# Kernel tuning notes

Measured on AMD Instinct MI355X. Metric: run time of the kernel, lower is better.

The kernel has to match this reference:

```python
import jax, jax.numpy as jnp
import numpy as np

N_NODES = 50000
N_EDGES = 800000
D_IN = 128
HID = [128, 64, 64]
N_CLASSES = 2
N_PROTO = 8
K = N_CLASSES * N_PROTO  # 16 = mlp_input_dim


def setup_inputs() -> dict:
    key = jax.random.key(0)
    ks = jax.random.split(key, 16)
    def lin(k, fi, fo):
        kw, kb = jax.random.split(k)
        s = 1.0 / np.sqrt(fi)
        return (jax.random.uniform(kw, (fi, fo), jnp.float32, -s, s),
                jax.random.uniform(kb, (fo,), jnp.float32, -s, s))
    W1, b1 = lin(ks[0], D_IN, HID[0])
    W2, b2 = lin(ks[1], HID[0], HID[1])
    W3, b3 = lin(ks[2], HID[1], HID[2])
    Wf0, bf0 = lin(ks[3], K, K // 2)
    Wf1, bf1 = lin(ks[4], K // 2, 1)
    return {
        'x': jax.random.normal(ks[5], (N_NODES, D_IN), jnp.float32),
        'edge_index': jax.random.randint(ks[6], (2, N_EDGES), 0, N_NODES, jnp.int64),
        'y': jax.random.randint(ks[7], (N_NODES,), 0, 2, jnp.int64),
        'W1': W1, 'b1': b1, 'W2': W2, 'b2': b2, 'W3': W3, 'b3': b3,
        'prototypes': jax.random.normal(ks[8], (N_CLASSES, N_PROTO, HID[2]), jnp.float32),
        'Wf0': Wf0, 'bf0': bf0, 'Wf1': Wf1, 'bf1': bf1,
    }


def reference(x, edge_index, y, W1, b1, W2, b2, W3, b3, prototypes, Wf0, bf0, Wf1, bf1):
    n = x.shape[0]
    loop = jnp.arange(n, dtype=edge_index.dtype)
    src = jnp.concatenate([edge_index[0], loop])  # A + I self loops (GCNConv default)
    dst = jnp.concatenate([edge_index[1], loop])
    deg = jax.ops.segment_sum(jnp.ones(src.shape[0], x.dtype), dst, num_segments=n)
    dinv = jax.lax.rsqrt(deg)  # deg >= 1 thanks to self loops
    enorm = dinv[src] * dinv[dst]  # sym-normalized edge weights

    def gcn(h, W, b):
        msg = (h @ W)[src] * enorm[:, None]  # gather + transform
        return jax.ops.segment_sum(msg, dst, num_segments=n) + b  # scatter-add

    h = jax.nn.relu(gcn(x, W1, b1))
    h = jax.nn.relu(gcn(h, W2, b2))
    h = jax.nn.relu(gcn(h, W3, b3))  # [n, 64]

    prot = prototypes.reshape(-1, prototypes.shape[-1])  # [K, 64]
    d2 = jnp.maximum(jnp.sum(h * h, -1, keepdims=True)
                     + jnp.sum(prot * prot, -1)[None, :]
                     - 2.0 * (h @ prot.T), 0.0)  # squared Euclidean [n, K]
    sim = jnp.log((d2 + 1.0) / (d2 + 1e-4))

    # MLPReadout, eval mode (dropout inactive), exact GELU like torch nn.GELU
    z = jax.nn.gelu(sim @ Wf0 + bf0, approximate=False)
    out = jax.nn.sigmoid(z @ Wf1 + bf1)
    return (out.squeeze(), y.astype(jnp.float32))
```

## Files before the change

### kernel.cpp

```cpp
#include <hip/hip_runtime.h>
#include <hip/hip_bf16.h>
#include <math.h>


typedef __attribute__((ext_vector_type(8))) short short8;
typedef __attribute__((ext_vector_type(4))) float f32x4;

#define BKT_SHIFT 5
#define BKT_NODES 32
#define EPB 2048
#define LCAP 1024
#define PREPN 28672
#define PREPB 112

__device__ __forceinline__ short f2bs(float x) {
    __hip_bfloat16 b = __float2bfloat16(x);
    return *reinterpret_cast<short*>(&b);
}
__device__ __forceinline__ float2 bpair(unsigned u) {
    float lo = __uint_as_float(u << 16);
    float hi = __uint_as_float(u & 0xffff0000u);
    return make_float2(lo, hi);
}
__device__ __forceinline__ unsigned packbf(float a, float b) {
    unsigned la = (unsigned)(unsigned short)f2bs(a);
    unsigned hb = (unsigned)(unsigned short)f2bs(b);
    return la | (hb << 16);
}

__device__ __forceinline__ void block_excl_scan(int* __restrict__ arr, int n, int t) {
    __shared__ int wsums[4];
    int lane = t & 63, wv = t >> 6;
    int carry = 0;
    for (int c0 = 0; c0 < n; c0 += 256) {
        int i = c0 + t;
        int v = (i < n) ? arr[i] : 0;
        int orig = v;
#pragma unroll
        for (int off = 1; off < 64; off <<= 1) {
            int u = __shfl_up(v, off, 64);
            if (lane >= off) v += u;
        }
        if (lane == 63) wsums[wv] = v;
        __syncthreads();
        int w0 = wsums[0], w1 = wsums[1], w2 = wsums[2], w3 = wsums[3];
        int woff = (wv > 0 ? w0 : 0) + (wv > 1 ? w1 : 0) + (wv > 2 ? w2 : 0);
        int tot = w0 + w1 + w2 + w3;
        __syncthreads();
        if (i < n) arr[i] = carry + woff + (v - orig);
        carry += tot;
    }
}


__global__ __launch_bounds__(256) void sort_local_kernel(const int* __restrict__ ei, int E,
                                                         int NB, int B,
                                                         int* __restrict__ glens,
                                                         int* __restrict__ gstart,
                                                         int* __restrict__ edge_sorted,
                                                         const float* __restrict__ W1,
                                                         const float* __restrict__ W2,
                                                         const float* __restrict__ W3,
                                                         __hip_bfloat16* __restrict__ Wp1,
                                                         __hip_bfloat16* __restrict__ Wp2,
                                                         __hip_bfloat16* __restrict__ Wp3) {
    int t = threadIdx.x;
    if ((int)blockIdx.x >= B) {
        int i = ((int)blockIdx.x - B) * 256 + t;
        if (i < 16384) {
            int k = i >> 7, n = i & 127;
            Wp1[(((k >> 3) * 128) + n) * 8 + (k & 7)] = __float2bfloat16(W1[i]);
        } else if (i < 24576) {
            int j = i - 16384;
            int k = j >> 6, n = j & 63;
            Wp2[(((k >> 3) * 64) + n) * 8 + (k & 7)] = __float2bfloat16(W2[j]);
        } else if (i < PREPN) {
            int j = i - 24576;
            int k = j >> 6, n = j & 63;
            Wp3[(((k >> 3) * 64) + n) * 8 + (k & 7)] = __float2bfloat16(W3[j]);
        }
        return;
    }
    extern __shared__ int lds[];
    int* hist  = lds;
    int* lbase = lds + NB;
    int* sortd = lds + 2 * NB;
    int blk = blockIdx.x;
    int e0 = blk * EPB;
    int cnt = E - e0;
    if (cnt > EPB) cnt = EPB;

    for (int i = t; i < NB; i += 256) hist[i] = 0;
    __syncthreads();
    for (int i = t; i < cnt; i += 256) {
        int dst = ei[E + e0 + i];
        atomicAdd(&hist[dst >> BKT_SHIFT], 1);
    }
    __syncthreads();
    for (int i = t; i < NB; i += 256) lbase[i] = hist[i];
    __syncthreads();
    block_excl_scan(lbase, NB, t);
    __syncthreads();
    for (int i = t; i < NB; i += 256) {
        glens[(size_t)blk * NB + i] = hist[i];
        gstart[(size_t)blk * NB + i] = lbase[i];
    }
    __syncthreads();
    for (int i = t; i < cnt; i += 256) {
        int src = ei[e0 + i];
        int dst = ei[E + e0 + i];
        int pos = atomicAdd(&lbase[dst >> BKT_SHIFT], 1);
        sortd[pos] = (src << BKT_SHIFT) | (dst & (BKT_NODES - 1));
    }
    __syncthreads();
    for (int i = t; i < cnt; i += 256) edge_sorted[e0 + i] = sortd[i];
}

__global__ __launch_bounds__(256) void csr_build_kernel(const int* __restrict__ edge_sorted,
                                                        const int* __restrict__ glens,
                                                        const int* __restrict__ gstart,
                                                        int NB, int B, int N,
                                                        int* __restrict__ row_beg,
                                                        int* __restrict__ row_end,
                                                        float* __restrict__ dinv,
                                                        int* __restrict__ csr) {
    __shared__ int lruns[512];
    __shared__ int loffs[512];
    __shared__ int sdeg[BKT_NODES];
    __shared__ int scur[BKT_NODES];
    __shared__ int raw[LCAP];
    __shared__ int srt[LCAP];
    int b = blockIdx.x;
    int t = threadIdx.x;

    for (int i = t; i < 512; i += 256) {
        int v = (i < B) ? glens[(size_t)i * NB + b] : 0;
        lruns[i] = v;
        loffs[i] = v;
    }
    if (t < BKT_NODES) sdeg[t] = 0;
    __syncthreads();
    block_excl_scan(loffs, B, t);
    __syncthreads();
    int cnt = loffs[B - 1] + lruns[B - 1];
    if (cnt > LCAP) cnt = LCAP;

    for (int r = t; r < B; r += 256) {
        int len = lruns[r];
        if (len) {
            int off = loffs[r];
            int st = r * EPB + gstart[(size_t)r * NB + b];
            for (int k = 0; k < len; ++k) {
                int p = off + k;
                if (p < LCAP) raw[p] = edge_sorted[st + k];
            }
        }
    }
    __syncthreads();

    for (int i = t; i < cnt; i += 256) atomicAdd(&sdeg[raw[i] & (BKT_NODES - 1)], 1);
    __syncthreads();
    int base = b * LCAP;
    if (t < BKT_NODES) {
        int ssum = 0;
        for (int i = 0; i < t; ++i) ssum += sdeg[i];
        scur[t] = ssum;
        int node = b * BKT_NODES + t;
        if (node < N) {
            row_beg[node] = base + ssum;
            row_end[node] = base + ssum + sdeg[t];
            dinv[node] = rsqrtf((float)(sdeg[t] + 1));
        }
    }
    __syncthreads();
    for (int i = t; i < cnt; i += 256) {
        int p = raw[i];
        int pos = atomicAdd(&scur[p & (BKT_NODES - 1)], 1);
        srt[pos] = p >> BKT_SHIFT;
    }
    __syncthreads();
    for (int i = t; i < cnt; i += 256) csr[base + i] = srt[i];
}


template <int DI, int DO, bool AF32>
__global__ __launch_bounds__(256) void mfma_gemm_kernel(const void* __restrict__ Av,
                                                        const __hip_bfloat16* __restrict__ Wp,
                                                        const float* __restrict__ dinv,
                                                        __hip_bfloat16* __restrict__ C, int N) {
    constexpr int NT = DO / 16;
    int t = threadIdx.x;
    int wave = t >> 6, lane = t & 63;
    int q = lane >> 4, l16 = lane & 15;
    int rbase = blockIdx.x * 64 + wave * 16;
    int row = rbase + l16;
    int rowc = row < N ? row : N - 1;

    f32x4 acc[NT];
#pragma unroll
    for (int i = 0; i < NT; ++i) acc[i] = (f32x4){0.f, 0.f, 0.f, 0.f};

#pragma unroll
    for (int kt = 0; kt < DI / 32; ++kt) {
        int k0 = kt * 32 + q * 8;
        short8 afrag;
        if (AF32) {
            const float* A = (const float*)Av;
            const float* ap = A + (size_t)rowc * DI + k0;
            float4 lo = *(const float4*)ap;
            float4 hi = *(const float4*)(ap + 4);
            afrag[0] = f2bs(lo.x); afrag[1] = f2bs(lo.y);
            afrag[2] = f2bs(lo.z); afrag[3] = f2bs(lo.w);
            afrag[4] = f2bs(hi.x); afrag[5] = f2bs(hi.y);
            afrag[6] = f2bs(hi.z); afrag[7] = f2bs(hi.w);
        } else {
            const __hip_bfloat16* A = (const __hip_bfloat16*)Av;
            afrag = *(const short8*)(A + (size_t)rowc * DI + k0);
        }
        const short8* wrow = (const short8*)(Wp + (size_t)(kt * 4 + q) * DO * 8);
#pragma unroll
        for (int tt = 0; tt < NT; ++tt) {
            short8 bfrag = wrow[tt * 16 + l16];
            acc[tt] = __builtin_amdgcn_mfma_f32_16x16x32_bf16(afrag, bfrag, acc[tt], 0, 0, 0);
        }
    }
#pragma unroll
    for (int r = 0; r < 4; ++r) {
        int gr = rbase + q * 4 + r;
        if (gr < N) {
            float dv = dinv[gr];
#pragma unroll
            for (int tt = 0; tt < NT; ++tt)
                C[(size_t)gr * DO + tt * 16 + l16] = __float2bfloat16(acc[tt][r] * dv);
        }
    }
}


__global__ __launch_bounds__(256) void agg128_kernel(const uint4* __restrict__ tmp,
                                                     const float* __restrict__ bias,
                                                     const float* __restrict__ dinv,
                                                     const int* __restrict__ row_beg,
                                                     const int* __restrict__ row_end,
                                                     const int* __restrict__ csr_src,
                                                     uint4* __restrict__ outp, int N) {
    int lane = threadIdx.x & 63;
    int q = lane >> 4, sub = lane & 15;
    int node = blockIdx.x * 4 + (threadIdx.x >> 6);
    if (node >= N) return;
    float dvi = dinv[node];
    float a0 = 0, a1 = 0, a2 = 0, a3 = 0, a4 = 0, a5 = 0, a6 = 0, a7 = 0;
    if (q == 0) {
        uint4 sv = tmp[(size_t)node * 16 + sub];
        float2 p0 = bpair(sv.x), p1 = bpair(sv.y), p2 = bpair(sv.z), p3 = bpair(sv.w);
        a0 = p0.x; a1 = p0.y; a2 = p1.x; a3 = p1.y;
        a4 = p2.x; a5 = p2.y; a6 = p3.x; a7 = p3.y;
    }
    int beg = row_beg[node], end = row_end[node];
    for (int j = beg; j < end; j += 64) {
        int m = end - j;
        if (m > 64) m = 64;
        int s = (lane < m) ? csr_src[j + lane] : 0;
        int iters = (m + 3) >> 2;
        for (int k = 0; k < iters; ++k) {
            int e = 4 * k + q;
            int ec = (e < m) ? e : 0;
            int sk = __shfl(s, ec, 64);
            uint4 v = tmp[(size_t)sk * 16 + sub];
            if (e < m) {
                float2 p0 = bpair(v.x), p1 = bpair(v.y), p2 = bpair(v.z), p3 = bpair(v.w);
                a0 += p0.x; a1 += p0.y; a2 += p1.x; a3 += p1.y;
                a4 += p2.x; a5 += p2.y; a6 += p3.x; a7 += p3.y;
            }
        }
    }
    a0 += __shfl_xor(a0, 16, 64); a1 += __shfl_xor(a1, 16, 64);
    a2 += __shfl_xor(a2, 16, 64); a3 += __shfl_xor(a3, 16, 64);
    a4 += __shfl_xor(a4, 16, 64); a5 += __shfl_xor(a5, 16, 64);
    a6 += __shfl_xor(a6, 16, 64); a7 += __shfl_xor(a7, 16, 64);
    a0 += __shfl_xor(a0, 32, 64); a1 += __shfl_xor(a1, 32, 64);
    a2 += __shfl_xor(a2, 32, 64); a3 += __shfl_xor(a3, 32, 64);
    a4 += __shfl_xor(a4, 32, 64); a5 += __shfl_xor(a5, 32, 64);
    a6 += __shfl_xor(a6, 32, 64); a7 += __shfl_xor(a7, 32, 64);
    if (q == 0) {
        float4 b0 = *(const float4*)&bias[sub * 8];
        float4 b1 = *(const float4*)&bias[sub * 8 + 4];
        uint4 o;
        o.x = packbf(fmaxf(dvi * a0 + b0.x, 0.f), fmaxf(dvi * a1 + b0.y, 0.f));
        o.y = packbf(fmaxf(dvi * a2 + b0.z, 0.f), fmaxf(dvi * a3 + b0.w, 0.f));
        o.z = packbf(fmaxf(dvi * a4 + b1.x, 0.f), fmaxf(dvi * a5 + b1.y, 0.f));
        o.w = packbf(fmaxf(dvi * a6 + b1.z, 0.f), fmaxf(dvi * a7 + b1.w, 0.f));
        outp[(size_t)node * 16 + sub] = o;
    }
}

__global__ __launch_bounds__(256) void agg64_kernel(const uint4* __restrict__ tmp,
                                                    const float* __restrict__ bias,
                                                    const float* __restrict__ dinv,
                                                    const int* __restrict__ row_beg,
                                                    const int* __restrict__ row_end,
                                                    const int* __restrict__ csr_src,
                                                    uint4* __restrict__ outp, int N) {
    int lane = threadIdx.x & 63;
    int o8 = lane >> 3, sub = lane & 7;
    int node = blockIdx.x * 4 + (threadIdx.x >> 6);
    if (node >= N) return;
    float dvi = dinv[node];
    float a0 = 0, a1 = 0, a2 = 0, a3 = 0, a4 = 0, a5 = 0, a6 = 0, a7 = 0;
    if (o8 == 0) {
        uint4 sv = tmp[(size_t)node * 8 + sub];
        float2 p0 = bpair(sv.x), p1 = bpair(sv.y), p2 = bpair(sv.z), p3 = bpair(sv.w);
        a0 = p0.x; a1 = p0.y; a2 = p1.x; a3 = p1.y;
        a4 = p2.x; a5 = p2.y; a6 = p3.x; a7 = p3.y;
    }
    int beg = row_beg[node], end = row_end[node];
    for (int j = beg; j < end; j += 64) {
        int m = end - j;
        if (m > 64) m = 64;
        int s = (lane < m) ? csr_src[j + lane] : 0;
        int iters = (m + 7) >> 3;
        for (int k = 0; k < iters; ++k) {
            int e = 8 * k + o8;
            int ec = (e < m) ? e : 0;
            int sk = __shfl(s, ec, 64);
            uint4 v = tmp[(size_t)sk * 8 + sub];
            if (e < m) {
                float2 p0 = bpair(v.x), p1 = bpair(v.y), p2 = bpair(v.z), p3 = bpair(v.w);
                a0 += p0.x; a1 += p0.y; a2 += p1.x; a3 += p1.y;
                a4 += p2.x; a5 += p2.y; a6 += p3.x; a7 += p3.y;
            }
        }
    }
    a0 += __shfl_xor(a0, 8, 64); a1 += __shfl_xor(a1, 8, 64);
    a2 += __shfl_xor(a2, 8, 64); a3 += __shfl_xor(a3, 8, 64);
    a4 += __shfl_xor(a4, 8, 64); a5 += __shfl_xor(a5, 8, 64);
    a6 += __shfl_xor(a6, 8, 64); a7 += __shfl_xor(a7, 8, 64);
    a0 += __shfl_xor(a0, 16, 64); a1 += __shfl_xor(a1, 16, 64);
    a2 += __shfl_xor(a2, 16, 64); a3 += __shfl_xor(a3, 16, 64);
    a4 += __shfl_xor(a4, 16, 64); a5 += __shfl_xor(a5, 16, 64);
    a6 += __shfl_xor(a6, 16, 64); a7 += __shfl_xor(a7, 16, 64);
    a0 += __shfl_xor(a0, 32, 64); a1 += __shfl_xor(a1, 32, 64);
    a2 += __shfl_xor(a2, 32, 64); a3 += __shfl_xor(a3, 32, 64);
    a4 += __shfl_xor(a4, 32, 64); a5 += __shfl_xor(a5, 32, 64);
    a6 += __shfl_xor(a6, 32, 64); a7 += __shfl_xor(a7, 32, 64);
    if (o8 == 0) {
        float4 b0 = *(const float4*)&bias[sub * 8];
        float4 b1 = *(const float4*)&bias[sub * 8 + 4];
        uint4 o;
        o.x = packbf(fmaxf(dvi * a0 + b0.x, 0.f), fmaxf(dvi * a1 + b0.y, 0.f));
        o.y = packbf(fmaxf(dvi * a2 + b0.z, 0.f), fmaxf(dvi * a3 + b0.w, 0.f));
        o.z = packbf(fmaxf(dvi * a4 + b1.x, 0.f), fmaxf(dvi * a5 + b1.y, 0.f));
        o.w = packbf(fmaxf(dvi * a6 + b1.z, 0.f), fmaxf(dvi * a7 + b1.w, 0.f));
        outp[(size_t)node * 8 + sub] = o;
    }
}


__global__ __launch_bounds__(256) void head_kernel(const unsigned* __restrict__ h,
                                                   const float* __restrict__ protos,
                                                   const float* __restrict__ Wf0,
                                                   const float* __restrict__ bf0,
                                                   const float* __restrict__ Wf1,
                                                   const float* __restrict__ bf1,
                                                   const int* __restrict__ y,
                                                   float* __restrict__ out, int N) {
    __shared__ float Hl[64 * 65];
    __shared__ float Pl[16 * 65];
    __shared__ float hh[64];
    __shared__ float pp[16];
    __shared__ float sim[64 * 17];
    __shared__ float Wf0l[128];
    __shared__ float bf0l[8];
    __shared__ float Wf1l[8];
    __shared__ float bf1l;
    int t = threadIdx.x;
    int n0 = blockIdx.x * 64;

    for (int idx = t; idx < 64 * 32; idx += 256) {
        int r = idx >> 5, c = idx & 31;
        int g = n0 + r;
        unsigned u = (g < N) ? h[(size_t)g * 32 + c] : 0u;
        float2 v = bpair(u);
        Hl[r * 65 + 2 * c] = v.x;
        Hl[r * 65 + 2 * c + 1] = v.y;
    }
    for (int idx = t; idx < 16 * 64; idx += 256) {
        int r = idx >> 6, c = idx & 63;
        Pl[r * 65 + c] = protos[idx];
    }
    if (t < 128) Wf0l[t] = Wf0[t];
    if (t < 8) { bf0l[t] = bf0[t]; Wf1l[t] = Wf1[t]; }
    if (t == 0) bf1l = bf1[0];
    __syncthreads();

    if (t < 64) {
        float s = 0.0f;
        for (int k = 0; k < 64; ++k) { float v = Hl[t * 65 + k]; s += v * v; }
        hh[t] = s;
    } else if (t < 80) {
        int p = t - 64;
        float s = 0.0f;
        for (int k = 0; k < 64; ++k) { float v = Pl[p * 65 + k]; s += v * v; }
        pp[p] = s;
    }
    __syncthreads();

    {
        int node = t & 63;
        int p4 = (t >> 6) * 4;
        float d0 = 0, d1 = 0, d2 = 0, d3 = 0;
        for (int k = 0; k < 64; ++k) {
            float hv = Hl[node * 65 + k];
            d0 += hv * Pl[(p4 + 0) * 65 + k];
            d1 += hv * Pl[(p4 + 1) * 65 + k];
            d2 += hv * Pl[(p4 + 2) * 65 + k];
            d3 += hv * Pl[(p4 + 3) * 65 + k];
        }
        float hhv = hh[node];
        float dd[4] = {d0, d1, d2, d3};
#pragma unroll
        for (int j = 0; j < 4; ++j) {
            float q = hhv + pp[p4 + j] - 2.0f * dd[j];
            q = q > 0.0f ? q : 0.0f;
            sim[node * 17 + p4 + j] = logf((q + 1.0f) / (q + 1e-4f));
        }
    }
    __syncthreads();

    if (t < 64) {
        int g = n0 + t;
        if (g < N) {
            float zacc = bf1l;
#pragma unroll
            for (int o = 0; o < 8; ++o) {
                float s = bf0l[o];
#pragma unroll
                for (int i2 = 0; i2 < 16; ++i2) s += sim[t * 17 + i2] * Wf0l[i2 * 8 + o];
                float gz = 0.5f * s * (1.0f + erff(s * 0.70710678118654752f));
                zacc += gz * Wf1l[o];
            }
            out[g] = 1.0f / (1.0f + expf(-zacc));
        }
    } else if (t < 128) {
        int g = n0 + (t - 64);
        if (g < N) out[N + g] = (float)y[g];
    }
}


extern "C" void kernel_launch(void* const* d_in, const int* in_sizes, int n_in,
                              void* d_out, int out_size, void* d_ws, size_t ws_size,
                              hipStream_t stream) {
    const float* x   = (const float*)d_in[0];
    const int*   ei  = (const int*)d_in[1];
    const int*   y   = (const int*)d_in[2];
    const float* W1  = (const float*)d_in[3];
    const float* b1  = (const float*)d_in[4];
    const float* W2  = (const float*)d_in[5];
    const float* b2  = (const float*)d_in[6];
    const float* W3  = (const float*)d_in[7];
    const float* b3  = (const float*)d_in[8];
    const float* pr  = (const float*)d_in[9];
    const float* Wf0 = (const float*)d_in[10];
    const float* bf0 = (const float*)d_in[11];
    const float* Wf1 = (const float*)d_in[12];
    const float* bf1 = (const float*)d_in[13];
    float* outp = (float*)d_out;

    const int N = in_sizes[2];
    const int E = in_sizes[1] / 2;
    const int NB = (N + BKT_NODES - 1) / BKT_NODES;
    const int B = (E + EPB - 1) / EPB;

    char* w = (char*)d_ws;
    auto carve = [&](size_t bytes) {
        char* p = w;
        w += (bytes + 511) & ~(size_t)511;
        return p;
    };
    int*   glens   = (int*)carve((size_t)B * NB * 4);
    int*   gstart  = (int*)carve((size_t)B * NB * 4);
    int*   esort   = (int*)carve((size_t)B * EPB * 4);
    int*   row_beg = (int*)carve((size_t)N * 4);
    int*   row_end = (int*)carve((size_t)N * 4);
    float* dinv    = (float*)carve((size_t)N * 4);
    int*   csr     = (int*)carve((size_t)NB * LCAP * 4);
    __hip_bfloat16* Wp1 = (__hip_bfloat16*)carve(16384 * 2);
    __hip_bfloat16* Wp2 = (__hip_bfloat16*)carve(8192 * 2);
    __hip_bfloat16* Wp3 = (__hip_bfloat16*)carve(4096 * 2);
    __hip_bfloat16* bufT = (__hip_bfloat16*)carve((size_t)N * 128 * 2);
    __hip_bfloat16* bufH = (__hip_bfloat16*)carve((size_t)N * 128 * 2);

    size_t sort_lds = (size_t)(2 * NB + EPB) * 4;

    sort_local_kernel<<<B + PREPB, 256, sort_lds, stream>>>(ei, E, NB, B, glens, gstart, esort,
                                                            W1, W2, W3, Wp1, Wp2, Wp3);
    csr_build_kernel<<<NB, 256, 0, stream>>>(esort, glens, gstart, NB, B, N,
                                             row_beg, row_end, dinv, csr);

    mfma_gemm_kernel<128, 128, true><<<(N + 63) / 64, 256, 0, stream>>>(x, Wp1, dinv, bufT, N);
    agg128_kernel<<<(N + 3) / 4, 256, 0, stream>>>((const uint4*)bufT, b1, dinv, row_beg, row_end,
                                                   csr, (uint4*)bufH, N);
    mfma_gemm_kernel<128, 64, false><<<(N + 63) / 64, 256, 0, stream>>>(bufH, Wp2, dinv, bufT, N);
    agg64_kernel<<<(N + 3) / 4, 256, 0, stream>>>((const uint4*)bufT, b2, dinv, row_beg, row_end,
                                                  csr, (uint4*)bufH, N);
    mfma_gemm_kernel<64, 64, false><<<(N + 63) / 64, 256, 0, stream>>>(bufH, Wp3, dinv, bufT, N);
    agg64_kernel<<<(N + 3) / 4, 256, 0, stream>>>((const uint4*)bufT, b3, dinv, row_beg, row_end,
                                                  csr, (uint4*)bufH, N);
    head_kernel<<<(N + 63) / 64, 256, 0, stream>>>((const unsigned*)bufH, pr, Wf0, bf0, Wf1, bf1,
                                                   y, outp, N);
}
```

Measured before the change: 246.1 us.

## Fuse GEMMs into aggregation kernels and overlap layer-1 GEMM with CSR build

The layer-1 GEMM now runs in the same launch as the CSR build, which lets it proceed without dinv; the source-side normalization moves into the first aggregation. The layer-2 and layer-3 transforms are fused into the preceding aggregation kernels as fp32 LDS matvecs, and the head is fused into the final aggregation. This drops kernel launches and the intermediate activation round trips through memory. The cost is that the small GEMMs move from MFMA to scalar FMA, with W2 and W3 read from global memory by every block, and the head now runs only 4 nodes per block with little parallelism.

Measured after the change: 317.4 us. 29.0% more time.

```diff
diff --git a/kernel.cpp b/kernel.cpp
--- a/kernel.cpp
+++ b/kernel.cpp
@@ -10,8 +10,6 @@
 #define BKT_NODES 32
 #define EPB 2048
 #define LCAP 1024
-#define PREPN 28672
-#define PREPB 112
 
 __device__ __forceinline__ short f2bs(float x) {
     __hip_bfloat16 b = __float2bfloat16(x);
@@ -21,11 +19,6 @@
     float lo = __uint_as_float(u << 16);
     float hi = __uint_as_float(u & 0xffff0000u);
     return make_float2(lo, hi);
-}
-__device__ __forceinline__ unsigned packbf(float a, float b) {
-    unsigned la = (unsigned)(unsigned short)f2bs(a);
-    unsigned hb = (unsigned)(unsigned short)f2bs(b);
-    return la | (hb << 16);
 }
 
 __device__ __forceinline__ void block_excl_scan(int* __restrict__ arr, int n, int t) {
@@ -53,31 +46,19 @@
 }
 
 
-__global__ __launch_bounds__(256) void sort_local_kernel(const int* __restrict__ ei, int E,
-                                                         int NB, int B,
-                                                         int* __restrict__ glens,
-                                                         int* __restrict__ gstart,
-                                                         int* __restrict__ edge_sorted,
-                                                         const float* __restrict__ W1,
-                                                         const float* __restrict__ W2,
-                                                         const float* __restrict__ W3,
-                                                         __hip_bfloat16* __restrict__ Wp1,
-                                                         __hip_bfloat16* __restrict__ Wp2,
-                                                         __hip_bfloat16* __restrict__ Wp3) {
+__global__ __launch_bounds__(256) void sort_w1_kernel(const int* __restrict__ ei, int E,
+                                                      int NB, int B,
+                                                      int* __restrict__ glens,
+                                                      int* __restrict__ gstart,
+                                                      int* __restrict__ edge_sorted,
+                                                      const float* __restrict__ W1,
+                                                      __hip_bfloat16* __restrict__ Wp1) {
     int t = threadIdx.x;
     if ((int)blockIdx.x >= B) {
         int i = ((int)blockIdx.x - B) * 256 + t;
         if (i < 16384) {
             int k = i >> 7, n = i & 127;
             Wp1[(((k >> 3) * 128) + n) * 8 + (k & 7)] = __float2bfloat16(W1[i]);
-        } else if (i < 24576) {
-            int j = i - 16384;
-            int k = j >> 6, n = j & 63;
-            Wp2[(((k >> 3) * 64) + n) * 8 + (k & 7)] = __float2bfloat16(W2[j]);
-        } else if (i < PREPN) {
-            int j = i - 24576;
-            int k = j >> 6, n = j & 63;
-            Wp3[(((k >> 3) * 64) + n) * 8 + (k & 7)] = __float2bfloat16(W3[j]);
         }
         return;
     }
@@ -116,14 +97,58 @@
     for (int i = t; i < cnt; i += 256) edge_sorted[e0 + i] = sortd[i];
 }
 
-__global__ __launch_bounds__(256) void csr_build_kernel(const int* __restrict__ edge_sorted,
+
+__global__ __launch_bounds__(256) void csr_gemm1_kernel(const int* __restrict__ edge_sorted,
                                                         const int* __restrict__ glens,
                                                         const int* __restrict__ gstart,
                                                         int NB, int B, int N,
                                                         int* __restrict__ row_beg,
                                                         int* __restrict__ row_end,
                                                         float* __restrict__ dinv,
-                                                        int* __restrict__ csr) {
+                                                        int* __restrict__ csr,
+                                                        const float* __restrict__ X,
+                                                        const __hip_bfloat16* __restrict__ Wp1,
+                                                        __hip_bfloat16* __restrict__ T1) {
+    int t = threadIdx.x;
+    if ((int)blockIdx.x >= NB) {
+        int bid = (int)blockIdx.x - NB;
+        int wave = t >> 6, lane = t & 63;
+        int q = lane >> 4, l16 = lane & 15;
+        int rbase = bid * 64 + wave * 16;
+        int row = rbase + l16;
+        int rowc = row < N ? row : N - 1;
+        f32x4 acc[8];
+#pragma unroll
+        for (int i = 0; i < 8; ++i) acc[i] = (f32x4){0.f, 0.f, 0.f, 0.f};
+#pragma unroll
+        for (int kt = 0; kt < 4; ++kt) {
+            int k0 = kt * 32 + q * 8;
+            const float* ap = X + (size_t)rowc * 128 + k0;
+            float4 lo = *(const float4*)ap;
+            float4 hi = *(const float4*)(ap + 4);
+            short8 afrag;
+            afrag[0] = f2bs(lo.x); afrag[1] = f2bs(lo.y);
+            afrag[2] = f2bs(lo.z); afrag[3] = f2bs(lo.w);
+            afrag[4] = f2bs(hi.x); afrag[5] = f2bs(hi.y);
+            afrag[6] = f2bs(hi.z); afrag[7] = f2bs(hi.w);
+            const short8* wrow = (const short8*)(Wp1 + (size_t)(kt * 4 + q) * 128 * 8);
+#pragma unroll
+            for (int tt = 0; tt < 8; ++tt) {
+                short8 bfrag = wrow[tt * 16 + l16];
+                acc[tt] = __builtin_amdgcn_mfma_f32_16x16x32_bf16(afrag, bfrag, acc[tt], 0, 0, 0);
+            }
+        }
+#pragma unroll
+        for (int r = 0; r < 4; ++r) {
+            int gr = rbase + q * 4 + r;
+            if (gr < N) {
+#pragma unroll
+                for (int tt = 0; tt < 8; ++tt)
+                    T1[(size_t)gr * 128 + tt * 16 + l16] = __float2bfloat16(acc[tt][r]);
+            }
+        }
+        return;
+    }
     __shared__ int lruns[512];
     __shared__ int loffs[512];
     __shared__ int sdeg[BKT_NODES];
@@ -131,7 +156,6 @@
     __shared__ int raw[LCAP];
     __shared__ int srt[LCAP];
     int b = blockIdx.x;
-    int t = threadIdx.x;
 
     for (int i = t; i < 512; i += 256) {
         int v = (i < B) ? glens[(size_t)i * NB + b] : 0;
@@ -157,7 +181,6 @@
         }
     }
     __syncthreads();
-
     for (int i = t; i < cnt; i += 256) atomicAdd(&sdeg[raw[i] & (BKT_NODES - 1)], 1);
     __syncthreads();
     int base = b * LCAP;
@@ -183,94 +206,46 @@
 }
 
 
-template <int DI, int DO, bool AF32>
-__global__ __launch_bounds__(256) void mfma_gemm_kernel(const void* __restrict__ Av,
-                                                        const __hip_bfloat16* __restrict__ Wp,
+__global__ __launch_bounds__(256) void agg128_g2_kernel(const uint4* __restrict__ T1,
+                                                        const float* __restrict__ b1,
                                                         const float* __restrict__ dinv,
-                                                        __hip_bfloat16* __restrict__ C, int N) {
-    constexpr int NT = DO / 16;
+                                                        const int* __restrict__ row_beg,
+                                                        const int* __restrict__ row_end,
+                                                        const int* __restrict__ csr,
+                                                        const float* __restrict__ W2,
+                                                        __hip_bfloat16* __restrict__ T2, int N) {
+    __shared__ float h1[4][128];
     int t = threadIdx.x;
-    int wave = t >> 6, lane = t & 63;
-    int q = lane >> 4, l16 = lane & 15;
-    int rbase = blockIdx.x * 64 + wave * 16;
-    int row = rbase + l16;
-    int rowc = row < N ? row : N - 1;
-
-    f32x4 acc[NT];
-#pragma unroll
-    for (int i = 0; i < NT; ++i) acc[i] = (f32x4){0.f, 0.f, 0.f, 0.f};
-
-#pragma unroll
-    for (int kt = 0; kt < DI / 32; ++kt) {
-        int k0 = kt * 32 + q * 8;
-        short8 afrag;
-        if (AF32) {
-            const float* A = (const float*)Av;
-            const float* ap = A + (size_t)rowc * DI + k0;
-            float4 lo = *(const float4*)ap;
-            float4 hi = *(const float4*)(ap + 4);
-            afrag[0] = f2bs(lo.x); afrag[1] = f2bs(lo.y);
-            afrag[2] = f2bs(lo.z); afrag[3] = f2bs(lo.w);
-            afrag[4] = f2bs(hi.x); afrag[5] = f2bs(hi.y);
-            afrag[6] = f2bs(hi.z); afrag[7] = f2bs(hi.w);
-        } else {
-            const __hip_bfloat16* A = (const __hip_bfloat16*)Av;
-            afrag = *(const short8*)(A + (size_t)rowc * DI + k0);
-        }
-        const short8* wrow = (const short8*)(Wp + (size_t)(kt * 4 + q) * DO * 8);
-#pragma unroll
-        for (int tt = 0; tt < NT; ++tt) {
-            short8 bfrag = wrow[tt * 16 + l16];
-            acc[tt] = __builtin_amdgcn_mfma_f32_16x16x32_bf16(afrag, bfrag, acc[tt], 0, 0, 0);
-        }
-    }
-#pragma unroll
-    for (int r = 0; r < 4; ++r) {
-        int gr = rbase + q * 4 + r;
-        if (gr < N) {
-            float dv = dinv[gr];
-#pragma unroll
-            for (int tt = 0; tt < NT; ++tt)
-                C[(size_t)gr * DO + tt * 16 + l16] = __float2bfloat16(acc[tt][r] * dv);
-        }
-    }
-}
-
-
-__global__ __launch_bounds__(256) void agg128_kernel(const uint4* __restrict__ tmp,
-                                                     const float* __restrict__ bias,
-                                                     const float* __restrict__ dinv,
-                                                     const int* __restrict__ row_beg,
-                                                     const int* __restrict__ row_end,
-                                                     const int* __restrict__ csr_src,
-                                                     uint4* __restrict__ outp, int N) {
-    int lane = threadIdx.x & 63;
+    int lane = t & 63, wv = t >> 6;
     int q = lane >> 4, sub = lane & 15;
-    int node = blockIdx.x * 4 + (threadIdx.x >> 6);
-    if (node >= N) return;
-    float dvi = dinv[node];
+    int node = blockIdx.x * 4 + wv;
+    int nd = node < N ? node : N - 1;
+    float dvi = dinv[nd];
     float a0 = 0, a1 = 0, a2 = 0, a3 = 0, a4 = 0, a5 = 0, a6 = 0, a7 = 0;
     if (q == 0) {
-        uint4 sv = tmp[(size_t)node * 16 + sub];
+        uint4 sv = T1[(size_t)nd * 16 + sub];
         float2 p0 = bpair(sv.x), p1 = bpair(sv.y), p2 = bpair(sv.z), p3 = bpair(sv.w);
-        a0 = p0.x; a1 = p0.y; a2 = p1.x; a3 = p1.y;
-        a4 = p2.x; a5 = p2.y; a6 = p3.x; a7 = p3.y;
-    }
-    int beg = row_beg[node], end = row_end[node];
+        a0 = dvi * p0.x; a1 = dvi * p0.y; a2 = dvi * p1.x; a3 = dvi * p1.y;
+        a4 = dvi * p2.x; a5 = dvi * p2.y; a6 = dvi * p3.x; a7 = dvi * p3.y;
+    }
+    int beg = row_beg[nd], end = row_end[nd];
     for (int j = beg; j < end; j += 64) {
         int m = end - j;
         if (m > 64) m = 64;
-        int s = (lane < m) ? csr_src[j + lane] : 0;
+        int s = 0;
+        float dv = 0.0f;
+        if (lane < m) { s = csr[j + lane]; dv = dinv[s]; }
         int iters = (m + 3) >> 2;
         for (int k = 0; k < iters; ++k) {
             int e = 4 * k + q;
             int ec = (e < m) ? e : 0;
             int sk = __shfl(s, ec, 64);
-            uint4 v = tmp[(size_t)sk * 16 + sub];
+            float dk = __shfl(dv, ec, 64);
+            uint4 v = T1[(size_t)sk * 16 + sub];
             if (e < m) {
                 float2 p0 = bpair(v.x), p1 = bpair(v.y), p2 = bpair(v.z), p3 = bpair(v.w);
-                a0 += p0.x; a1 += p0.y; a2 += p1.x; a3 += p1.y;
-                a4 += p2.x; a5 += p2.y; a6 += p3.x; a7 += p3.y;
+                a0 += dk * p0.x; a1 += dk * p0.y; a2 += dk * p1.x; a3 += dk * p1.y;
+                a4 += dk * p2.x; a5 += dk * p2.y; a6 += dk * p3.x; a7 += dk * p3.y;
             }
         }
     }
@@ -283,47 +258,60 @@
     a4 += __shfl_xor(a4, 32, 64); a5 += __shfl_xor(a5, 32, 64);
     a6 += __shfl_xor(a6, 32, 64); a7 += __shfl_xor(a7, 32, 64);
     if (q == 0) {
-        float4 b0 = *(const float4*)&bias[sub * 8];
-        float4 b1 = *(const float4*)&bias[sub * 8 + 4];
-        uint4 o;
-        o.x = packbf(fmaxf(dvi * a0 + b0.x, 0.f), fmaxf(dvi * a1 + b0.y, 0.f));
-        o.y = packbf(fmaxf(dvi * a2 + b0.z, 0.f), fmaxf(dvi * a3 + b0.w, 0.f));
-        o.z = packbf(fmaxf(dvi * a4 + b1.x, 0.f), fmaxf(dvi * a5 + b1.y, 0.f));
-        o.w = packbf(fmaxf(dvi * a6 + b1.z, 0.f), fmaxf(dvi * a7 + b1.w, 0.f));
-        outp[(size_t)node * 16 + sub] = o;
-    }
-}
-
-__global__ __launch_bounds__(256) void agg64_kernel(const uint4* __restrict__ tmp,
-                                                    const float* __restrict__ bias,
-                                                    const float* __restrict__ dinv,
-                                                    const int* __restrict__ row_beg,
-                                                    const int* __restrict__ row_end,
-                                                    const int* __restrict__ csr_src,
-                                                    uint4* __restrict__ outp, int N) {
-    int lane = threadIdx.x & 63;
+        float4 bb0 = *(const float4*)&b1[sub * 8];
+        float4 bb1 = *(const float4*)&b1[sub * 8 + 4];
+        h1[wv][sub * 8 + 0] = fmaxf(dvi * a0 + bb0.x, 0.f);
+        h1[wv][sub * 8 + 1] = fmaxf(dvi * a1 + bb0.y, 0.f);
+        h1[wv][sub * 8 + 2] = fmaxf(dvi * a2 + bb0.z, 0.f);
+        h1[wv][sub * 8 + 3] = fmaxf(dvi * a3 + bb0.w, 0.f);
+        h1[wv][sub * 8 + 4] = fmaxf(dvi * a4 + bb1.x, 0.f);
+        h1[wv][sub * 8 + 5] = fmaxf(dvi * a5 + bb1.y, 0.f);
+        h1[wv][sub * 8 + 6] = fmaxf(dvi * a6 + bb1.z, 0.f);
+        h1[wv][sub * 8 + 7] = fmaxf(dvi * a7 + bb1.w, 0.f);
+    }
+    __syncthreads();
+    int nd2 = t >> 6, c = t & 63;
+    float acc = 0.0f;
+#pragma unroll 4
+    for (int k = 0; k < 128; ++k) acc += h1[nd2][k] * W2[k * 64 + c];
+    int gn = blockIdx.x * 4 + nd2;
+    if (gn < N) T2[(size_t)gn * 64 + c] = __float2bfloat16(dinv[gn] * acc);
+}
+
+
+__global__ __launch_bounds__(256) void agg64_g3_kernel(const uint4* __restrict__ T2,
+                                                       const float* __restrict__ b2,
+                                                       const float* __restrict__ dinv,
+                                                       const int* __restrict__ row_beg,
+                                                       const int* __restrict__ row_end,
+                                                       const int* __restrict__ csr,
+                                                       const float* __restrict__ W3,
+                                                       __hip_bfloat16* __restrict__ T3, int N) {
+    __shared__ float h2[4][64];
+    int t = threadIdx.x;
+    int lane = t & 63, wv = t >> 6;
     int o8 = lane >> 3, sub = lane & 7;
-    int node = blockIdx.x * 4 + (threadIdx.x >> 6);
-    if (node >= N) return;
-    float dvi = dinv[node];
+    int node = blockIdx.x * 4 + wv;
+    int nd = node < N ? node : N - 1;
+    float dvi = dinv[nd];
     float a0 = 0, a1 = 0, a2 = 0, a3 = 0, a4 = 0, a5 = 0, a6 = 0, a7 = 0;
     if (o8 == 0) {
-        uint4 sv = tmp[(size_t)node * 8 + sub];
+        uint4 sv = T2[(size_t)nd * 8 + sub];
         float2 p0 = bpair(sv.x), p1 = bpair(sv.y), p2 = bpair(sv.z), p3 = bpair(sv.w);
         a0 = p0.x; a1 = p0.y; a2 = p1.x; a3 = p1.y;
         a4 = p2.x; a5 = p2.y; a6 = p3.x; a7 = p3.y;
     }
-    int beg = row_beg[node], end = row_end[node];
+    int beg = row_beg[nd], end = row_end[nd];
     for (int j = beg; j < end; j += 64) {
         int m = end - j;
         if (m > 64) m = 64;
-        int s = (lane < m) ? csr_src[j + lane] : 0;
+        int s = (lane < m) ? csr[j + lane] : 0;
         int iters = (m + 7) >> 3;
         for (int k = 0; k < iters; ++k) {
             int e = 8 * k + o8;
             int ec = (e < m) ? e : 0;
             int sk = __shfl(s, ec, 64);
-            uint4 v = tmp[(size_t)sk * 8 + sub];
+            uint4 v = T2[(size_t)sk * 8 + sub];
             if (e < m) {
                 float2 p0 = bpair(v.x), p1 = bpair(v.y), p2 = bpair(v.z), p3 = bpair(v.w);
                 a0 += p0.x; a1 += p0.y; a2 += p1.x; a3 += p1.y;
@@ -331,119 +319,142 @@
             }
         }
     }
-    a0 += __shfl_xor(a0, 8, 64); a1 += __shfl_xor(a1, 8, 64);
-    a2 += __shfl_xor(a2, 8, 64); a3 += __shfl_xor(a3, 8, 64);
-    a4 += __shfl_xor(a4, 8, 64); a5 += __shfl_xor(a5, 8, 64);
-    a6 += __shfl_xor(a6, 8, 64); a7 += __shfl_xor(a7, 8, 64);
-    a0 += __shfl_xor(a0, 16, 64); a1 += __shfl_xor(a1, 16, 64);
-    a2 += __shfl_xor(a2, 16, 64); a3 += __shfl_xor(a3, 16, 64);
-    a4 += __shfl_xor(a4, 16, 64); a5 += __shfl_xor(a5, 16, 64);
-    a6 += __shfl_xor(a6, 16, 64); a7 += __shfl_xor(a7, 16, 64);
-    a0 += __shfl_xor(a0, 32, 64); a1 += __shfl_xor(a1, 32, 64);
-    a2 += __shfl_xor(a2, 32, 64); a3 += __shfl_xor(a3, 32, 64);
-    a4 += __shfl_xor(a4, 32, 64); a5 += __shfl_xor(a5, 32, 64);
-    a6 += __shfl_xor(a6, 32, 64); a7 += __shfl_xor(a7, 32, 64);
+#pragma unroll
+    for (int off = 8; off <= 32; off <<= 1) {
+        a0 += __shfl_xor(a0, off, 64); a1 += __shfl_xor(a1, off, 64);
+        a2 += __shfl_xor(a2, off, 64); a3 += __shfl_xor(a3, off, 64);
+        a4 += __shfl_xor(a4, off, 64); a5 += __shfl_xor(a5, off, 64);
+        a6 += __shfl_xor(a6, off, 64); a7 += __shfl_xor(a7, off, 64);
+    }
     if (o8 == 0) {
-        float4 b0 = *(const float4*)&bias[sub * 8];
-        float4 b1 = *(const float4*)&bias[sub * 8 + 4];
-        uint4 o;
-        o.x = packbf(fmaxf(dvi * a0 + b0.x, 0.f), fmaxf(dvi * a1 + b0.y, 0.f));
-        o.y = packbf(fmaxf(dvi * a2 + b0.z, 0.f), fmaxf(dvi * a3 + b0.w, 0.f));
-        o.z = packbf(fmaxf(dvi * a4 + b1.x, 0.f), fmaxf(dvi * a5 + b1.y, 0.f));
-        o.w = packbf(fmaxf(dvi * a6 + b1.z, 0.f), fmaxf(dvi * a7 + b1.w, 0.f));
-        outp[(size_t)node * 8 + sub] = o;
-    }
-}
-
-
-__global__ __launch_bounds__(256) void head_kernel(const unsigned* __restrict__ h,
-                                                   const float* __restrict__ protos,
-                                                   const float* __restrict__ Wf0,
-                                                   const float* __restrict__ bf0,
-                                                   const float* __restrict__ Wf1,
-                                                   const float* __restrict__ bf1,
-                                                   const int* __restrict__ y,
-                                                   float* __restrict__ out, int N) {
-    __shared__ float Hl[64 * 65];
-    __shared__ float Pl[16 * 65];
-    __shared__ float hh[64];
+        float4 bb0 = *(const float4*)&b2[sub * 8];
+        float4 bb1 = *(const float4*)&b2[sub * 8 + 4];
+        h2[wv][sub * 8 + 0] = fmaxf(dvi * a0 + bb0.x, 0.f);
+        h2[wv][sub * 8 + 1] = fmaxf(dvi * a1 + bb0.y, 0.f);
+        h2[wv][sub * 8 + 2] = fmaxf(dvi * a2 + bb0.z, 0.f);
+        h2[wv][sub * 8 + 3] = fmaxf(dvi * a3 + bb0.w, 0.f);
+        h2[wv][sub * 8 + 4] = fmaxf(dvi * a4 + bb1.x, 0.f);
+        h2[wv][sub * 8 + 5] = fmaxf(dvi * a5 + bb1.y, 0.f);
+        h2[wv][sub * 8 + 6] = fmaxf(dvi * a6 + bb1.z, 0.f);
+        h2[wv][sub * 8 + 7] = fmaxf(dvi * a7 + bb1.w, 0.f);
+    }
+    __syncthreads();
+    int nd2 = t >> 6, c = t & 63;
+    float acc = 0.0f;
+#pragma unroll 4
+    for (int k = 0; k < 64; ++k) acc += h2[nd2][k] * W3[k * 64 + c];
+    int gn = blockIdx.x * 4 + nd2;
+    if (gn < N) T3[(size_t)gn * 64 + c] = __float2bfloat16(dinv[gn] * acc);
+}
+
+
+__global__ __launch_bounds__(256) void agg64_head_kernel(const uint4* __restrict__ T3,
+                                                         const float* __restrict__ b3,
+                                                         const float* __restrict__ dinv,
+                                                         const int* __restrict__ row_beg,
+                                                         const int* __restrict__ row_end,
+                                                         const int* __restrict__ csr,
+                                                         const float* __restrict__ protos,
+                                                         const float* __restrict__ Wf0,
+                                                         const float* __restrict__ bf0,
+                                                         const float* __restrict__ Wf1,
+                                                         const float* __restrict__ bf1,
+                                                         const int* __restrict__ y,
+                                                         float* __restrict__ out, int N) {
+    __shared__ float h3[4][65];
+    __shared__ float Pl[16][65];
+    __shared__ float hh[4];
     __shared__ float pp[16];
-    __shared__ float sim[64 * 17];
-    __shared__ float Wf0l[128];
-    __shared__ float bf0l[8];
-    __shared__ float Wf1l[8];
-    __shared__ float bf1l;
+    __shared__ float sim[4][16];
     int t = threadIdx.x;
-    int n0 = blockIdx.x * 64;
-
-    for (int idx = t; idx < 64 * 32; idx += 256) {
-        int r = idx >> 5, c = idx & 31;
-        int g = n0 + r;
-        unsigned u = (g < N) ? h[(size_t)g * 32 + c] : 0u;
-        float2 v = bpair(u);
-        Hl[r * 65 + 2 * c] = v.x;
-        Hl[r * 65 + 2 * c + 1] = v.y;
-    }
-    for (int idx = t; idx < 16 * 64; idx += 256) {
-        int r = idx >> 6, c = idx & 63;
-        Pl[r * 65 + c] = protos[idx];
-    }
-    if (t < 128) Wf0l[t] = Wf0[t];
-    if (t < 8) { bf0l[t] = bf0[t]; Wf1l[t] = Wf1[t]; }
-    if (t == 0) bf1l = bf1[0];
-    __syncthreads();
-
+    int lane = t & 63, wv = t >> 6;
+    int o8 = lane >> 3, sub = lane & 7;
+    int node = blockIdx.x * 4 + wv;
+    int nd = node < N ? node : N - 1;
+    float dvi = dinv[nd];
+
+    for (int idx = t; idx < 1024; idx += 256) Pl[idx >> 6][idx & 63] = protos[idx];
+
+    float a0 = 0, a1 = 0, a2 = 0, a3 = 0, a4 = 0, a5 = 0, a6 = 0, a7 = 0;
+    if (o8 == 0) {
+        uint4 sv = T3[(size_t)nd * 8 + sub];
+        float2 p0 = bpair(sv.x), p1 = bpair(sv.y), p2 = bpair(sv.z), p3 = bpair(sv.w);
+        a0 = p0.x; a1 = p0.y; a2 = p1.x; a3 = p1.y;
+        a4 = p2.x; a5 = p2.y; a6 = p3.x; a7 = p3.y;
+    }
+    int beg = row_beg[nd], end = row_end[nd];
+    for (int j = beg; j < end; j += 64) {
+        int m = end - j;
+        if (m > 64) m = 64;
+        int s = (lane < m) ? csr[j + lane] : 0;
+        int iters = (m + 7) >> 3;
+        for (int k = 0; k < iters; ++k) {
+            int e = 8 * k + o8;
+            int ec = (e < m) ? e : 0;
+            int sk = __shfl(s, ec, 64);
+            uint4 v = T3[(size_t)sk * 8 + sub];
+            if (e < m) {
+                float2 p0 = bpair(v.x), p1 = bpair(v.y), p2 = bpair(v.z), p3 = bpair(v.w);
+                a0 += p0.x; a1 += p0.y; a2 += p1.x; a3 += p1.y;
+                a4 += p2.x; a5 += p2.y; a6 += p3.x; a7 += p3.y;
+            }
+        }
+    }
+#pragma unroll
+    for (int off = 8; off <= 32; off <<= 1) {
+        a0 += __shfl_xor(a0, off, 64); a1 += __shfl_xor(a1, off, 64);
+        a2 += __shfl_xor(a2, off, 64); a3 += __shfl_xor(a3, off, 64);
+        a4 += __shfl_xor(a4, off, 64); a5 += __shfl_xor(a5, off, 64);
+        a6 += __shfl_xor(a6, off, 64); a7 += __shfl_xor(a7, off, 64);
+    }
+    if (o8 == 0) {
+        float4 bb0 = *(const float4*)&b3[sub * 8];
+        float4 bb1 = *(const float4*)&b3[sub * 8 + 4];
+        h3[wv][sub * 8 + 0] = fmaxf(dvi * a0 + bb0.x, 0.f);
+        h3[wv][sub * 8 + 1] = fmaxf(dvi * a1 + bb0.y, 0.f);
+        h3[wv][sub * 8 + 2] = fmaxf(dvi * a2 + bb0.z, 0.f);
+        h3[wv][sub * 8 + 3] = fmaxf(dvi * a3 + bb0.w, 0.f);
+        h3[wv][sub * 8 + 4] = fmaxf(dvi * a4 + bb1.x, 0.f);
+        h3[wv][sub * 8 + 5] = fmaxf(dvi * a5 + bb1.y, 0.f);
+        h3[wv][sub * 8 + 6] = fmaxf(dvi * a6 + bb1.z, 0.f);
+        h3[wv][sub * 8 + 7] = fmaxf(dvi * a7 + bb1.w, 0.f);
+    }
+    __syncthreads();
+    if (t < 4) {
+        float s = 0.0f;
+        for (int k = 0; k < 64; ++k) { float v = h3[t][k]; s += v * v; }
+        hh[t] = s;
+    } else if (t >= 8 && t < 24) {
+        int p = t - 8;
+        float s = 0.0f;
+        for (int k = 0; k < 64; ++k) { float v = Pl[p][k]; s += v * v; }
+        pp[p] = s;
+    }
+    __syncthreads();
     if (t < 64) {
-        float s = 0.0f;
-        for (int k = 0; k < 64; ++k) { float v = Hl[t * 65 + k]; s += v * v; }
-        hh[t] = s;
-    } else if (t < 80) {
-        int p = t - 64;
-        float s = 0.0f;
-        for (int k = 0; k < 64; ++k) { float v = Pl[p * 65 + k]; s += v * v; }
-        pp[p] = s;
-    }
-    __syncthreads();
-
-    {
-        int node = t & 63;
-        int p4 = (t >> 6) * 4;
-        float d0 = 0, d1 = 0, d2 = 0, d3 = 0;
-        for (int k = 0; k < 64; ++k) {
-            float hv = Hl[node * 65 + k];
-            d0 += hv * Pl[(p4 + 0) * 65 + k];
-            d1 += hv * Pl[(p4 + 1) * 65 + k];
-            d2 += hv * Pl[(p4 + 2) * 65 + k];
-            d3 += hv * Pl[(p4 + 3) * 65 + k];
-        }
-        float hhv = hh[node];
-        float dd[4] = {d0, d1, d2, d3};
-#pragma unroll
-        for (int j = 0; j < 4; ++j) {
-            float q = hhv + pp[p4 + j] - 2.0f * dd[j];
-            q = q > 0.0f ? q : 0.0f;
-            sim[node * 17 + p4 + j] = logf((q + 1.0f) / (q + 1e-4f));
-        }
-    }
-    __syncthreads();
-
-    if (t < 64) {
-        int g = n0 + t;
+        int n2 = t >> 4, p = t & 15;
+        float d = 0.0f;
+        for (int k = 0; k < 64; ++k) d += h3[n2][k] * Pl[p][k];
+        float q2 = hh[n2] + pp[p] - 2.0f * d;
+        q2 = q2 > 0.0f ? q2 : 0.0f;
+        sim[n2][p] = logf((q2 + 1.0f) / (q2 + 1e-4f));
+    }
+    __syncthreads();
+    if (t < 4) {
+        int g = blockIdx.x * 4 + t;
         if (g < N) {
-            float zacc = bf1l;
+            float zacc = bf1[0];
 #pragma unroll
             for (int o = 0; o < 8; ++o) {
-                float s = bf0l[o];
-#pragma unroll
-                for (int i2 = 0; i2 < 16; ++i2) s += sim[t * 17 + i2] * Wf0l[i2 * 8 + o];
+                float s = bf0[o];
+#pragma unroll
+                for (int i2 = 0; i2 < 16; ++i2) s += sim[t][i2] * Wf0[i2 * 8 + o];
                 float gz = 0.5f * s * (1.0f + erff(s * 0.70710678118654752f));
-                zacc += gz * Wf1l[o];
+                zacc += gz * Wf1[o];
             }
             out[g] = 1.0f / (1.0f + expf(-zacc));
-        }
-    } else if (t < 128) {
-        int g = n0 + (t - 64);
-        if (g < N) out[N + g] = (float)y[g];
+            out[N + g] = (float)y[g];
+        }
     }
 }
 
@@ -486,27 +497,24 @@
     float* dinv    = (float*)carve((size_t)N * 4);
     int*   csr     = (int*)carve((size_t)NB * LCAP * 4);
     __hip_bfloat16* Wp1 = (__hip_bfloat16*)carve(16384 * 2);
-    __hip_bfloat16* Wp2 = (__hip_bfloat16*)carve(8192 * 2);
-    __hip_bfloat16* Wp3 = (__hip_bfloat16*)carve(4096 * 2);
-    __hip_bfloat16* bufT = (__hip_bfloat16*)carve((size_t)N * 128 * 2);
-    __hip_bfloat16* bufH = (__hip_bfloat16*)carve((size_t)N * 128 * 2);
+    __hip_bfloat16* T1  = (__hip_bfloat16*)carve((size_t)N * 128 * 2);
+    __hip_bfloat16* T2  = (__hip_bfloat16*)carve((size_t)N * 64 * 2);
+    __hip_bfloat16* T3  = (__hip_bfloat16*)carve((size_t)N * 64 * 2);
 
     size_t sort_lds = (size_t)(2 * NB + EPB) * 4;
 
-    sort_local_kernel<<<B + PREPB, 256, sort_lds, stream>>>(ei, E, NB, B, glens, gstart, esort,
-                                                            W1, W2, W3, Wp1, Wp2, Wp3);
-    csr_build_kernel<<<NB, 256, 0, stream>>>(esort, glens, gstart, NB, B, N,
-                                             row_beg, row_end, dinv, csr);
-
-    mfma_gemm_kernel<128, 128, true><<<(N + 63) / 64, 256, 0, stream>>>(x, Wp1, dinv, bufT, N);
-    agg128_kernel<<<(N + 3) / 4, 256, 0, stream>>>((const uint4*)bufT, b1, dinv, row_beg, row_end,
-                                                   csr, (uint4*)bufH, N);
-    mfma_gemm_kernel<128, 64, false><<<(N + 63) / 64, 256, 0, stream>>>(bufH, Wp2, dinv, bufT, N);
-    agg64_kernel<<<(N + 3) / 4, 256, 0, stream>>>((const uint4*)bufT, b2, dinv, row_beg, row_end,
-                                                  csr, (uint4*)bufH, N);
-    mfma_gemm_kernel<64, 64, false><<<(N + 63) / 64, 256, 0, stream>>>(bufH, Wp3, dinv, bufT, N);
-    agg64_kernel<<<(N + 3) / 4, 256, 0, stream>>>((const uint4*)bufT, b3, dinv, row_beg, row_end,
-                                                  csr, (uint4*)bufH, N);
-    head_kernel<<<(N + 63) / 64, 256, 0, stream>>>((const unsigned*)bufH, pr, Wf0, bf0, Wf1, bf1,
-                                                   y, outp, N);
-}
+    const int gemm1_blocks = (N + 63) / 64;
+    const int agg_blocks = (N + 3) / 4;
+
+    sort_w1_kernel<<<B + 64, 256, sort_lds, stream>>>(ei, E, NB, B, glens, gstart, esort,
+                                                      W1, Wp1);
+    csr_gemm1_kernel<<<NB + gemm1_blocks, 256, 0, stream>>>(esort, glens, gstart, NB, B, N,
+                                                            row_beg, row_end, dinv, csr,
+                                                            x, Wp1, T1);
+    agg128_g2_kernel<<<agg_blocks, 256, 0, stream>>>((const uint4*)T1, b1, dinv, row_beg, row_end,
+                                                     csr, W2, T2, N);
+    agg64_g3_kernel<<<agg_blocks, 256, 0, stream>>>((const uint4*)T2, b2, dinv, row_beg, row_end,
+                                                    csr, W3, T3, N);
+    agg64_head_kernel<<<agg_blocks, 256, 0, stream>>>((const uint4*)T3, b3, dinv, row_beg, row_end,
+                                                      csr, pr, Wf0, bf0, Wf1, bf1, y, outp, N);
+}
```
